# Optimization experiments

Measured on AMD Instinct MI355X. Metric: run time of the kernel, lower is better.

The kernel has to match this reference:

```python
import jax, jax.numpy as jnp
import numpy as np

B, D = 4096, 512
TOPK_NEG = 1024
TEMP = 0.01
LOSS_WEIGHT = 1.0
NEG_INF_MASK = 1e9
NUM_CLASSES = 1000


def _l2_normalize(x):
    # F.normalize(x, dim=1, p=2): x / max(||x||_2, eps)
    n = jnp.sqrt(jnp.sum(x * x, axis=1, keepdims=True))
    return x / jnp.maximum(n, 1e-12)


def setup_inputs() -> dict:
    key = jax.random.key(0)
    k1, k2, k3 = jax.random.split(key, 3)
    feat = jax.random.normal(k1, (B, D), dtype=jnp.float32)
    feat_old = jax.random.normal(k2, (B, D), dtype=jnp.float32)
    targets = jax.random.randint(k3, (B,), 0, NUM_CLASSES, dtype=jnp.int64)
    return {"feat": feat, "feat_old": feat_old, "targets": targets}


def reference(feat, feat_old, targets):
    fn = _l2_normalize(feat)                      # [B, D]
    fo = jax.lax.stop_gradient(_l2_normalize(feat_old))  # detached old feats

    # masks: same-label pairs (includes diagonal), used to suppress negatives
    masks = (targets[:, None] == targets[None, :]).astype(fn.dtype)  # [B, B]

    # positive logit: <feat_new_i, feat_old_i>  (the bmm in torch)
    logits_pos = jnp.sum(fn * fo, axis=1, keepdims=True)             # [B, 1]

    # negatives: new-to-old and new-to-new similarity, same-label masked out
    logits_n2o = fn @ fo.T - masks * NEG_INF_MASK                    # [B, B]
    logits_n2n = fn @ fn.T - masks * NEG_INF_MASK                    # [B, B]

    neg_n2o = jax.lax.top_k(logits_n2o, TOPK_NEG)[0]                 # [B, K]
    neg_n2n = jax.lax.top_k(logits_n2n, TOPK_NEG)[0]                 # [B, K]

    logits_all = jnp.concatenate([logits_pos, neg_n2o, neg_n2n], axis=1) / TEMP

    # CrossEntropyLoss with target class 0 for every row, mean reduction
    lse = jax.nn.logsumexp(logits_all, axis=1)
    loss = jnp.mean(lse - logits_all[:, 0]) * LOSS_WEIGHT
    return loss
```

## Files before the change

### kernel.cpp

```cpp
#include <hip/hip_runtime.h>
#include <hip/hip_bf16.h>

#define BB 4096
#define DD 512

typedef unsigned short u16;
typedef unsigned int u32;
typedef signed char s8;

using f32x4 = __attribute__((ext_vector_type(4))) float;
using i32x4 = __attribute__((ext_vector_type(4))) int;

constexpr float QS = 400.0f;
constexpr float CEXP = 144.26950408889634f;
constexpr float CEXPQ = CEXP / (QS * QS);
constexpr float EOFF = 64.0f - 144.26950408889634f;
constexpr float LN2 = 0.6931471805599453f;
constexpr float LSE_BASE = 100.0f - 64.0f * 0.6931471805599453f;

__device__ __forceinline__ float wave_sum(float v) {
#pragma unroll
  for (int m = 1; m < 64; m <<= 1) v += __shfl_xor(v, m);
  return v;
}

__device__ __forceinline__ void gload16(const void* g, const void* l) {
  __builtin_amdgcn_global_load_lds(
      (const __attribute__((address_space(1))) void*)g,
      (__attribute__((address_space(3))) void*)(const_cast<void*>(l)), 16, 0, 0);
}

__device__ __forceinline__ void barrier_raw() {
  asm volatile("" ::: "memory");
  __builtin_amdgcn_s_barrier();
  asm volatile("" ::: "memory");
}

__device__ __forceinline__ u32 q4(float a, float b, float c, float d, float s) {
  const int qa = (int)rintf(fminf(fmaxf(a * s, -127.0f), 127.0f));
  const int qb = (int)rintf(fminf(fmaxf(b * s, -127.0f), 127.0f));
  const int qc = (int)rintf(fminf(fmaxf(c * s, -127.0f), 127.0f));
  const int qd = (int)rintf(fminf(fmaxf(d * s, -127.0f), 127.0f));
  return (qa & 0xff) | ((qb & 0xff) << 8) | ((qc & 0xff) << 16) | ((qd & 0xff) << 24);
}

__global__ __launch_bounds__(256) void k_norm(const float* __restrict__ feat,
                                              const float* __restrict__ feat_old,
                                              s8* __restrict__ fn8, s8* __restrict__ fo8,
                                              float* __restrict__ pos) {
  const int i = blockIdx.x * 4 + (threadIdx.x >> 6);
  const int t = threadIdx.x & 63;
  const float4 x0 = *(const float4*)(feat + (size_t)i * DD + t * 4);
  const float4 x1 = *(const float4*)(feat + (size_t)i * DD + 256 + t * 4);
  const float4 y0 = *(const float4*)(feat_old + (size_t)i * DD + t * 4);
  const float4 y1 = *(const float4*)(feat_old + (size_t)i * DD + 256 + t * 4);
  float sx = x0.x * x0.x + x0.y * x0.y + x0.z * x0.z + x0.w * x0.w +
             x1.x * x1.x + x1.y * x1.y + x1.z * x1.z + x1.w * x1.w;
  float sy = y0.x * y0.x + y0.y * y0.y + y0.z * y0.z + y0.w * y0.w +
             y1.x * y1.x + y1.y * y1.y + y1.z * y1.z + y1.w * y1.w;
  float sxy = x0.x * y0.x + x0.y * y0.y + x0.z * y0.z + x0.w * y0.w +
              x1.x * y1.x + x1.y * y1.y + x1.z * y1.z + x1.w * y1.w;
  sx = wave_sum(sx);
  sy = wave_sum(sy);
  sxy = wave_sum(sxy);
  const float inx = 1.0f / fmaxf(sqrtf(sx), 1e-12f);
  const float iny = 1.0f / fmaxf(sqrtf(sy), 1e-12f);
  const float sxq = inx * QS, syq = iny * QS;
  u32* px0 = (u32*)(fn8 + (size_t)i * DD + t * 4);
  u32* px1 = (u32*)(fn8 + (size_t)i * DD + 256 + t * 4);
  u32* py0 = (u32*)(fo8 + (size_t)i * DD + t * 4);
  u32* py1 = (u32*)(fo8 + (size_t)i * DD + 256 + t * 4);
  *px0 = q4(x0.x, x0.y, x0.z, x0.w, sxq);
  *px1 = q4(x1.x, x1.y, x1.z, x1.w, sxq);
  *py0 = q4(y0.x, y0.y, y0.z, y0.w, syq);
  *py1 = q4(y1.x, y1.y, y1.z, y1.w, syq);
  if (t == 0) pos[i] = sxy * inx * iny;
}

__global__ __launch_bounds__(512, 2) void k_fused(const s8* __restrict__ fn8,
                                                  const s8* __restrict__ fo8,
                                                  const int* __restrict__ tgt,
                                                  float* __restrict__ partial) {
  __shared__ __align__(16) s8 lA[2][256 * 64];
  __shared__ __align__(16) s8 lB1[2][128 * 64];
  __shared__ __align__(16) s8 lB2[2][128 * 64];

  const int tid = threadIdx.x;
  const int lane = tid & 63;
  const int wid = tid >> 6;
  const int wr = wid & 3;
  const int sel = wid >> 2;
  const int lrow = lane & 15;
  const int lkg = lane >> 4;

  const int flat = blockIdx.x;
  const int swz = (flat & 7) * 64 + (flat >> 3);
  const int mt = swz >> 5, nt = swz & 31;
  const int row0 = mt * 256, jb = nt * 128;

  const int crow = lane >> 2;
  const int cofs = 16 * ((lane & 3) ^ ((lane >> 3) & 3));

  auto stageA = [&](s8* dst, int kk) {
#pragma unroll
    for (int i = 0; i < 2; ++i) {
      const int c = wid * 2 + i;
      gload16(fn8 + (size_t)(row0 + c * 16 + crow) * DD + kk + cofs, dst + c * 1024);
    }
  };
  auto stageB = [&](s8* d1, s8* d2, int kk) {
    const int c = wid;
    gload16(fo8 + (size_t)(jb + c * 16 + crow) * DD + kk + cofs, d1 + c * 1024);
    gload16(fn8 + (size_t)(jb + c * 16 + crow) * DD + kk + cofs, d2 + c * 1024);
  };

  i32x4 acc[4][8];
#pragma unroll
  for (int a = 0; a < 4; ++a)
#pragma unroll
    for (int b = 0; b < 8; ++b) acc[a][b] = (i32x4)(0);

  stageA(lA[0], 0);
  stageB(lB1[0], lB2[0], 0);

  for (int t = 0; t < 8; ++t) {
    const int cur = t & 1, nxt = cur ^ 1;
    const s8* cA = lA[cur];
    const s8* cB = sel ? lB2[cur] : lB1[cur];

    if (t < 7) {
      stageA(lA[nxt], (t + 1) * 64);
      asm volatile("s_waitcnt vmcnt(2)" ::: "memory");
    } else {
      asm volatile("s_waitcnt vmcnt(0)" ::: "memory");
    }
    barrier_raw();

    i32x4 av[4], bv[8];
#pragma unroll
    for (int f = 0; f < 4; ++f) {
      const int ar = wr * 64 + f * 16 + lrow;
      av[f] = *(const i32x4*)(cA + ar * 64 + ((lkg ^ ((ar >> 1) & 3)) * 16));
    }
#pragma unroll
    for (int f = 0; f < 8; ++f) {
      const int br = f * 16 + lrow;
      bv[f] = *(const i32x4*)(cB + br * 64 + ((lkg ^ ((br >> 1) & 3)) * 16));
    }
    if (t < 7) stageB(lB1[nxt], lB2[nxt], (t + 1) * 64);
    __builtin_amdgcn_s_setprio(1);
#pragma unroll
    for (int fr = 0; fr < 4; ++fr)
#pragma unroll
      for (int fc = 0; fc < 8; ++fc)
        acc[fr][fc] = __builtin_amdgcn_mfma_i32_16x16x64_i8(av[fr], bv[fc], acc[fr][fc], 0, 0, 0);
    __builtin_amdgcn_s_setprio(0);
    barrier_raw();
  }

  const bool isN2O = (sel == 0);
  int tc[8];
#pragma unroll
  for (int fc = 0; fc < 8; ++fc) tc[fc] = tgt[jb + fc * 16 + lrow];
  float* rsum = (float*)lA;
#pragma unroll
  for (int fr = 0; fr < 4; ++fr) {
#pragma unroll
    for (int reg = 0; reg < 4; ++reg) {
      const int gr = row0 + wr * 64 + fr * 16 + lkg * 4 + reg;
      const int trv = tgt[gr];
      float s = 0.0f;
#pragma unroll
      for (int fc = 0; fc < 8; ++fc) {
        const int gc = jb + fc * 16 + lrow;
        const float p = __builtin_amdgcn_exp2f(fmaf((float)acc[fr][fc][reg], CEXPQ, EOFF));
        const bool keep = (trv != tc[fc]) || (isN2O && gr == gc);
        s += keep ? p : 0.0f;
      }
      s += __shfl_xor(s, 1);
      s += __shfl_xor(s, 2);
      s += __shfl_xor(s, 4);
      s += __shfl_xor(s, 8);
      if (lrow == 0) rsum[sel * 256 + wr * 64 + fr * 16 + lkg * 4 + reg] = s;
    }
  }
  asm volatile("s_waitcnt lgkmcnt(0)" ::: "memory");
  barrier_raw();
  if (tid < 256) {
    const float v = rsum[tid] + rsum[256 + tid];
    partial[(size_t)(row0 + tid) * 32 + nt] = v;
  }
}

__global__ __launch_bounds__(256) void k_final(const float* __restrict__ partial,
                                               const float* __restrict__ pos,
                                               float* __restrict__ bsum) {
  const int t = threadIdx.x;
  const int r = blockIdx.x * 128 + (t >> 1);
  const int half = t & 1;
  const float4* p = (const float4*)(partial + (size_t)r * 32 + half * 16);
  float v = 0.0f;
#pragma unroll
  for (int q = 0; q < 4; ++q) {
    const float4 a = p[q];
    v += (a.x + a.y) + (a.z + a.w);
  }
  v += __shfl_xor(v, 1);
  float contrib = (half == 0)
                      ? (LSE_BASE + __builtin_amdgcn_logf(v) * LN2 - 100.0f * pos[r])
                      : 0.0f;
  contrib = wave_sum(contrib);
  __shared__ float red[4];
  if ((t & 63) == 0) red[t >> 6] = contrib;
  __syncthreads();
  if (t == 0) bsum[blockIdx.x] = (red[0] + red[1]) + (red[2] + red[3]);
}

__global__ __launch_bounds__(64) void k_mean(const float* __restrict__ bsum,
                                             float* __restrict__ out) {
  float s = (threadIdx.x < 32) ? bsum[threadIdx.x] : 0.0f;
  s = wave_sum(s);
  if (threadIdx.x == 0) out[0] = s * (1.0f / (float)BB);
}

extern "C" void kernel_launch(void* const* d_in, const int* in_sizes, int n_in,
                              void* d_out, int out_size, void* d_ws, size_t ws_size,
                              hipStream_t stream) {
  const float* feat = (const float*)d_in[0];
  const float* feat_old = (const float*)d_in[1];
  const int* targets = (const int*)d_in[2];
  float* out = (float*)d_out;
  char* ws = (char*)d_ws;

  s8* fn8 = (s8*)ws;
  s8* fo8 = (s8*)(ws + 2u * 1024 * 1024);
  float* pos = (float*)(ws + 4u * 1024 * 1024);
  float* partial = (float*)(ws + 4u * 1024 * 1024 + 16 * 1024);
  float* bsum = (float*)(ws + 4u * 1024 * 1024 + 544 * 1024);

  k_norm<<<BB / 4, 256, 0, stream>>>(feat, feat_old, fn8, fo8, pos);
  k_fused<<<512, 512, 0, stream>>>(fn8, fo8, targets, partial);
  k_final<<<32, 256, 0, stream>>>(partial, pos, bsum);
  k_mean<<<1, 64, 0, stream>>>(bsum, out);
}
```

Baseline: 42.46 us.

## Shrink fused GEMM tile to 128 rows and split warps 2x4 over rows and columns

The fused similarity kernel goes from 256-row tiles with 8 warps each owning a 64x128 slab to 128-row tiles with warps arranged 2x4, each computing 64x64. The grid doubles to 1024 blocks, accumulator registers are halved, launch bounds ask for 4 blocks per CU, and the A and B staging loads are issued together before the wait. The aim is better occupancy, more latency hiding and smaller LDS per block. The cost is lower data reuse per block, more global traffic for the B operand, and a four-way reduction of row sums at the end.

```diff
diff --git a/kernel.cpp b/kernel.cpp
--- a/kernel.cpp
+++ b/kernel.cpp
@@ -77,102 +77,101 @@
   if (t == 0) pos[i] = sxy * inx * iny;
 }
 
-__global__ __launch_bounds__(512, 2) void k_fused(const s8* __restrict__ fn8,
+__global__ __launch_bounds__(512, 4) void k_fused(const s8* __restrict__ fn8,
                                                   const s8* __restrict__ fo8,
                                                   const int* __restrict__ tgt,
                                                   float* __restrict__ partial) {
-  __shared__ __align__(16) s8 lA[2][256 * 64];
-  __shared__ __align__(16) s8 lB1[2][128 * 64];
-  __shared__ __align__(16) s8 lB2[2][128 * 64];
+  __shared__ __align__(16) s8 lA[2][128 * 64];
+  __shared__ __align__(16) s8 lB[2][256 * 64];
 
   const int tid = threadIdx.x;
   const int lane = tid & 63;
   const int wid = tid >> 6;
-  const int wr = wid & 3;
-  const int sel = wid >> 2;
+  const int wm = wid >> 2;
+  const int wn = wid & 3;
   const int lrow = lane & 15;
   const int lkg = lane >> 4;
 
   const int flat = blockIdx.x;
-  const int swz = (flat & 7) * 64 + (flat >> 3);
+  const int swz = (flat & 7) * 128 + (flat >> 3);
   const int mt = swz >> 5, nt = swz & 31;
-  const int row0 = mt * 256, jb = nt * 128;
+  const int row0 = mt * 128, jb = nt * 128;
 
   const int crow = lane >> 2;
   const int cofs = 16 * ((lane & 3) ^ ((lane >> 3) & 3));
 
   auto stageA = [&](s8* dst, int kk) {
+    gload16(fn8 + (size_t)(row0 + wid * 16 + crow) * DD + kk + cofs, dst + wid * 1024);
+  };
+  auto stageB = [&](s8* dst, int kk) {
 #pragma unroll
     for (int i = 0; i < 2; ++i) {
       const int c = wid * 2 + i;
-      gload16(fn8 + (size_t)(row0 + c * 16 + crow) * DD + kk + cofs, dst + c * 1024);
+      const s8* src = (c < 8) ? (fo8 + (size_t)(jb + c * 16 + crow) * DD + kk + cofs)
+                              : (fn8 + (size_t)(jb + (c - 8) * 16 + crow) * DD + kk + cofs);
+      gload16(src, dst + c * 1024);
     }
   };
-  auto stageB = [&](s8* d1, s8* d2, int kk) {
-    const int c = wid;
-    gload16(fo8 + (size_t)(jb + c * 16 + crow) * DD + kk + cofs, d1 + c * 1024);
-    gload16(fn8 + (size_t)(jb + c * 16 + crow) * DD + kk + cofs, d2 + c * 1024);
-  };
-
-  i32x4 acc[4][8];
+
+  i32x4 acc[4][4];
 #pragma unroll
   for (int a = 0; a < 4; ++a)
 #pragma unroll
-    for (int b = 0; b < 8; ++b) acc[a][b] = (i32x4)(0);
+    for (int b = 0; b < 4; ++b) acc[a][b] = (i32x4)(0);
 
   stageA(lA[0], 0);
-  stageB(lB1[0], lB2[0], 0);
+  stageB(lB[0], 0);
 
   for (int t = 0; t < 8; ++t) {
     const int cur = t & 1, nxt = cur ^ 1;
     const s8* cA = lA[cur];
-    const s8* cB = sel ? lB2[cur] : lB1[cur];
+    const s8* cB = lB[cur];
 
     if (t < 7) {
       stageA(lA[nxt], (t + 1) * 64);
-      asm volatile("s_waitcnt vmcnt(2)" ::: "memory");
+      stageB(lB[nxt], (t + 1) * 64);
+      asm volatile("s_waitcnt vmcnt(3)" ::: "memory");
     } else {
       asm volatile("s_waitcnt vmcnt(0)" ::: "memory");
     }
     barrier_raw();
 
-    i32x4 av[4], bv[8];
+    i32x4 av[4], bv[4];
 #pragma unroll
     for (int f = 0; f < 4; ++f) {
-      const int ar = wr * 64 + f * 16 + lrow;
+      const int ar = wm * 64 + f * 16 + lrow;
       av[f] = *(const i32x4*)(cA + ar * 64 + ((lkg ^ ((ar >> 1) & 3)) * 16));
     }
 #pragma unroll
-    for (int f = 0; f < 8; ++f) {
-      const int br = f * 16 + lrow;
+    for (int f = 0; f < 4; ++f) {
+      const int br = wn * 64 + f * 16 + lrow;
       bv[f] = *(const i32x4*)(cB + br * 64 + ((lkg ^ ((br >> 1) & 3)) * 16));
     }
-    if (t < 7) stageB(lB1[nxt], lB2[nxt], (t + 1) * 64);
     __builtin_amdgcn_s_setprio(1);
 #pragma unroll
     for (int fr = 0; fr < 4; ++fr)
 #pragma unroll
-      for (int fc = 0; fc < 8; ++fc)
+      for (int fc = 0; fc < 4; ++fc)
         acc[fr][fc] = __builtin_amdgcn_mfma_i32_16x16x64_i8(av[fr], bv[fc], acc[fr][fc], 0, 0, 0);
     __builtin_amdgcn_s_setprio(0);
     barrier_raw();
   }
 
-  const bool isN2O = (sel == 0);
-  int tc[8];
-#pragma unroll
-  for (int fc = 0; fc < 8; ++fc) tc[fc] = tgt[jb + fc * 16 + lrow];
+  const bool isN2O = (wn < 2);
+  int tc[4];
+#pragma unroll
+  for (int fc = 0; fc < 4; ++fc) tc[fc] = tgt[jb + (wn & 1) * 64 + fc * 16 + lrow];
   float* rsum = (float*)lA;
 #pragma unroll
   for (int fr = 0; fr < 4; ++fr) {
 #pragma unroll
     for (int reg = 0; reg < 4; ++reg) {
-      const int gr = row0 + wr * 64 + fr * 16 + lkg * 4 + reg;
+      const int gr = row0 + wm * 64 + fr * 16 + lkg * 4 + reg;
       const int trv = tgt[gr];
       float s = 0.0f;
 #pragma unroll
-      for (int fc = 0; fc < 8; ++fc) {
-        const int gc = jb + fc * 16 + lrow;
+      for (int fc = 0; fc < 4; ++fc) {
+        const int gc = jb + (wn & 1) * 64 + fc * 16 + lrow;
         const float p = __builtin_amdgcn_exp2f(fmaf((float)acc[fr][fc][reg], CEXPQ, EOFF));
         const bool keep = (trv != tc[fc]) || (isN2O && gr == gc);
         s += keep ? p : 0.0f;
@@ -181,13 +180,15 @@
       s += __shfl_xor(s, 2);
       s += __shfl_xor(s, 4);
       s += __shfl_xor(s, 8);
-      if (lrow == 0) rsum[sel * 256 + wr * 64 + fr * 16 + lkg * 4 + reg] = s;
+      if (lrow == 0) rsum[(wm * 4 + wn) * 64 + fr * 16 + lkg * 4 + reg] = s;
     }
   }
   asm volatile("s_waitcnt lgkmcnt(0)" ::: "memory");
   barrier_raw();
-  if (tid < 256) {
-    const float v = rsum[tid] + rsum[256 + tid];
+  if (tid < 128) {
+    const int wmg = tid >> 6, rl = tid & 63;
+    const float v = rsum[(wmg * 4 + 0) * 64 + rl] + rsum[(wmg * 4 + 1) * 64 + rl] +
+                    rsum[(wmg * 4 + 2) * 64 + rl] + rsum[(wmg * 4 + 3) * 64 + rl];
     partial[(size_t)(row0 + tid) * 32 + nt] = v;
   }
 }
@@ -239,7 +240,7 @@
   float* bsum = (float*)(ws + 4u * 1024 * 1024 + 544 * 1024);
 
   k_norm<<<BB / 4, 256, 0, stream>>>(feat, feat_old, fn8, fo8, pos);
-  k_fused<<<512, 512, 0, stream>>>(fn8, fo8, targets, partial);
+  k_fused<<<1024, 512, 0, stream>>>(fn8, fo8, targets, partial);
   k_final<<<32, 256, 0, stream>>>(partial, pos, bsum);
   k_mean<<<1, 64, 0, stream>>>(bsum, out);
 }
```

Result: no change. 42.61 us (+0.3%).
